# Performance work log

Measured on AMD Instinct MI355X. Metric: run time of the kernel, lower is better.

Reference implementation:

```python
import jax, jax.numpy as jnp
import numpy as np

# module config (matches init_kwargs)
NUM_CHIPS = 8
EPC = 8                 # experts_per_chip
E = 64                  # n_routed_experts = NUM_CHIPS * EPC
K = 4                   # num_experts_per_tok
META = 8                # metadata_len
M = 1024                # max_dispatched_tokens_per_expert
S = 512                 # seq_len_per_chip
H = 2048                # hidden_dim


def setup_inputs() -> dict:
    key = jax.random.key(0)
    k1, k2, k3 = jax.random.split(key, 3)
    x = jax.random.normal(k1, (NUM_CHIPS, S, H), jnp.float32)
    weights = jax.random.normal(k2, (NUM_CHIPS, S, K), jnp.float32)
    indices = jax.random.randint(k3, (NUM_CHIPS, S, K), 0, E, dtype=jnp.int32)
    return {"x": x, "weights": weights, "indices": indices}


def _local_ranks(f):
    # f: (S*K,) expert ids for one chip, in loop order (token-major, topk-minor).
    # rank[i] = number of earlier entries routed to the same expert.
    oh = (f[:, None] == jnp.arange(E)[None, :]).astype(jnp.int32)  # (SK, E)
    csum = jnp.cumsum(oh, axis=0)
    return jnp.take_along_axis(csum, f[:, None], axis=1)[:, 0] - 1


def reference(x, weights, indices):
    C, S_, K_ = indices.shape
    f = indices.reshape(C, S_ * K_)  # (C, SK) routed expert per dispatch entry

    # per-(chip, expert) token counts, then exclusive prefix-sum over chips -> base offsets
    counts = jax.vmap(lambda fi: jnp.zeros((E,), jnp.int32).at[fi].add(1))(f)  # (C, E)
    cum = jnp.cumsum(counts, axis=0)
    offset_base = jnp.concatenate([jnp.zeros((1, E), jnp.int32), cum[:-1]], axis=0)
    tokens_per_expert = cum[-1].reshape(NUM_CHIPS, EPC).astype(jnp.int32)

    # destination slot within each expert buffer = base offset + within-chip arrival rank
    rank = jax.vmap(_local_ranks)(f)                                 # (C, SK)
    dst = jnp.take_along_axis(offset_base, f, axis=1) + rank         # (C, SK)
    # expert_chip*EPC + expert_within_chip == routed_expert, so flat buffer row = f*M + dst
    slot = (f * M + dst).reshape(-1)                                 # (C*SK,)

    # scatter token hidden states
    x_entries = jnp.broadcast_to(x[:, :, None, :], (C, S_, K_, H)).reshape(-1, H)
    dispatched = (jnp.zeros((E * M, H), jnp.float32)
                  .at[slot].set(x_entries)
                  .reshape(NUM_CHIPS, EPC, M, H))

    # scatter metadata rows [chip, token, topk_idx, expert, int(weight), 0...]
    chip_ids = jnp.broadcast_to(jnp.arange(C)[:, None, None], (C, S_, K_)).reshape(-1)
    tok_ids = jnp.broadcast_to(jnp.arange(S_)[None, :, None], (C, S_, K_)).reshape(-1)
    k_ids = jnp.broadcast_to(jnp.arange(K_)[None, None, :], (C, S_, K_)).reshape(-1)
    w_int = weights.reshape(-1).astype(jnp.int32)  # original writes float into int32 buffer (truncates)
    meta_rows = jnp.stack([chip_ids, tok_ids, k_ids, f.reshape(-1), w_int], axis=1).astype(jnp.int32)
    meta_rows = jnp.concatenate(
        [meta_rows, jnp.zeros((meta_rows.shape[0], META - 5), jnp.int32)], axis=1)
    metadata = (jnp.full((E * M, META), -1, jnp.int32)
                .at[slot].set(meta_rows)
                .reshape(NUM_CHIPS, EPC, M, META))

    return dispatched, metadata, tokens_per_expert
```

## Files before the change

kernel.cpp:

```cpp
#include <hip/hip_runtime.h>

#define NUM_CHIPS 8
#define EPC 8
#define E_EXPERTS 64
#define TOPK 4
#define META 8
#define M_CAP 1024
#define SEQ 512
#define HID 2048
#define SK (SEQ * TOPK)
#define ROWS (E_EXPERTS * M_CAP)

#define DISP_SZ ((size_t)ROWS * HID)
#define META_OFF DISP_SZ
#define TOK_OFF (DISP_SZ + (size_t)ROWS * META)

#define WS_INV 0
#define WS_CNT (ROWS)
#define WS_OFB (ROWS + 512)
#define WS_TOT (ROWS + 1024)

typedef float vfloat4 __attribute__((ext_vector_type(4)));

__global__ __launch_bounds__(256) void count_kernel(const int* __restrict__ idx,
                                                    int* __restrict__ ws) {
    const int c = blockIdx.x;
    const int t = threadIdx.x;
    __shared__ __align__(16) unsigned char f[SK];
    __shared__ int partial[4][E_EXPERTS];

    const int* ic = idx + c * SK;
    for (int i = t; i < SK; i += 256) f[i] = (unsigned char)ic[i];
    __syncthreads();

    const int e = t & 63;
    const int q = t >> 6;
    const unsigned eb = (unsigned)e;
    const unsigned* fw = (const unsigned*)f;
    int cnt = 0;
    for (int w = q * 128; w < q * 128 + 128; ++w) {
        unsigned v = fw[w];
        cnt += ((v & 0xffu) == eb);
        cnt += (((v >> 8) & 0xffu) == eb);
        cnt += (((v >> 16) & 0xffu) == eb);
        cnt += ((v >> 24) == eb);
    }
    partial[q][e] = cnt;
    __syncthreads();
    if (q == 0) {
        int s = partial[0][e] + partial[1][e] + partial[2][e] + partial[3][e];
        ws[WS_CNT + c * E_EXPERTS + e] = s;
    }
}

__global__ void prefix_kernel(int* __restrict__ ws, float* __restrict__ out) {
    const int e = threadIdx.x;
    int base = 0;
    for (int c = 0; c < NUM_CHIPS; ++c) {
        ws[WS_OFB + c * E_EXPERTS + e] = base;
        base += ws[WS_CNT + c * E_EXPERTS + e];
    }
    ws[WS_TOT + e] = base;
    out[TOK_OFF + e] = (float)base;
}

__global__ __launch_bounds__(256) void rank_kernel(const int* __restrict__ idx,
                                                   int* __restrict__ ws) {
    const int c = blockIdx.x;
    const int t = threadIdx.x;
    __shared__ __align__(16) unsigned char f[SK];
    __shared__ int partial[4][E_EXPERTS];

    const int* ic = idx + c * SK;
    for (int i = t; i < SK; i += 256) f[i] = (unsigned char)ic[i];
    __syncthreads();

    const int e = t & 63;
    const int q = t >> 6;
    const unsigned eb = (unsigned)e;
    const unsigned* fw = (const unsigned*)f;
    int cnt = 0;
    for (int w = q * 128; w < q * 128 + 128; ++w) {
        unsigned v = fw[w];
        cnt += ((v & 0xffu) == eb);
        cnt += (((v >> 8) & 0xffu) == eb);
        cnt += (((v >> 16) & 0xffu) == eb);
        cnt += ((v >> 24) == eb);
    }
    partial[q][e] = cnt;
    __syncthreads();

    int base = ws[WS_OFB + c * E_EXPERTS + e];
    for (int qq = 0; qq < q; ++qq) base += partial[qq][e];

    int* inv = ws + WS_INV;
    for (int i = q * 512; i < q * 512 + 512; ++i) {
        if ((int)f[i] == e) {
            inv[e * M_CAP + base] = c * SK + i;
            ++base;
        }
    }
}

__global__ __launch_bounds__(256) void fill_kernel(const float* __restrict__ x,
                                                   const float* __restrict__ wts,
                                                   const int* __restrict__ ws,
                                                   float* __restrict__ out) {
    const int row = blockIdx.x;
    const int e = row >> 10;
    const int p = row & (M_CAP - 1);
    const int t = threadIdx.x;

    const int total = ws[WS_TOT + e];
    vfloat4* d4 = (vfloat4*)(out + (size_t)row * HID);
    float* meta = out + META_OFF + (size_t)row * META;

    if (p < total) {
        const int entry = ws[WS_INV + row];
        const int c = entry >> 11;
        const int i = entry & (SK - 1);
        const int tok = i >> 2;
        const int k = i & 3;
        const vfloat4* s4 = (const vfloat4*)(x + ((size_t)(c * SEQ + tok)) * HID);
        vfloat4 v0 = s4[t];
        vfloat4 v1 = s4[t + 256];
        __builtin_nontemporal_store(v0, d4 + t);
        __builtin_nontemporal_store(v1, d4 + t + 256);
        if (t < META) {
            float mv;
            if (t == 0)      mv = (float)c;
            else if (t == 1) mv = (float)tok;
            else if (t == 2) mv = (float)k;
            else if (t == 3) mv = (float)e;
            else if (t == 4) mv = (float)((int)wts[(c * SEQ + tok) * TOPK + k]);
            else             mv = 0.0f;
            meta[t] = mv;
        }
    } else {
        vfloat4 z = (vfloat4)(0.0f);
        __builtin_nontemporal_store(z, d4 + t);
        __builtin_nontemporal_store(z, d4 + t + 256);
        if (t < META) meta[t] = -1.0f;
    }
}

extern "C" void kernel_launch(void* const* d_in, const int* in_sizes, int n_in,
                              void* d_out, int out_size, void* d_ws, size_t ws_size,
                              hipStream_t stream) {
    const float* x   = (const float*)d_in[0];
    const float* wts = (const float*)d_in[1];
    const int* idx   = (const int*)d_in[2];
    float* out = (float*)d_out;
    int* ws = (int*)d_ws;

    count_kernel<<<NUM_CHIPS, 256, 0, stream>>>(idx, ws);
    prefix_kernel<<<1, 64, 0, stream>>>(ws, out);
    rank_kernel<<<NUM_CHIPS, 256, 0, stream>>>(idx, ws);
    fill_kernel<<<ROWS, 256, 0, stream>>>(x, wts, ws, out);
}
```

Measured before the change: 600.8 us.

## Zero-fill dispatch buffer with memset and launch copy blocks only for routed entries

```diff
diff --git a/kernel.cpp b/kernel.cpp
--- a/kernel.cpp
+++ b/kernel.cpp
@@ -10,15 +10,17 @@
 #define HID 2048
 #define SK (SEQ * TOPK)
 #define ROWS (E_EXPERTS * M_CAP)
+#define NENTRIES (NUM_CHIPS * SK)
 
 #define DISP_SZ ((size_t)ROWS * HID)
 #define META_OFF DISP_SZ
 #define TOK_OFF (DISP_SZ + (size_t)ROWS * META)
 
-#define WS_INV 0
-#define WS_CNT (ROWS)
-#define WS_OFB (ROWS + 512)
-#define WS_TOT (ROWS + 1024)
+#define WS_CNT 0
+#define WS_OFB 512
+#define WS_TOT 1024
+#define WS_GB  1088
+#define WS_DENSE 1152
 
 typedef float vfloat4 __attribute__((ext_vector_type(4)));
 
@@ -54,6 +56,7 @@
 }
 
 __global__ void prefix_kernel(int* __restrict__ ws, float* __restrict__ out) {
+    __shared__ int tot[E_EXPERTS];
     const int e = threadIdx.x;
     int base = 0;
     for (int c = 0; c < NUM_CHIPS; ++c) {
@@ -61,7 +64,12 @@
         base += ws[WS_CNT + c * E_EXPERTS + e];
     }
     ws[WS_TOT + e] = base;
+    tot[e] = base;
     out[TOK_OFF + e] = (float)base;
+    __syncthreads();
+    int g = 0;
+    for (int j = 0; j < e; ++j) g += tot[j];
+    ws[WS_GB + e] = g;
 }
 
 __global__ __launch_bounds__(256) void rank_kernel(const int* __restrict__ idx,
@@ -90,57 +98,57 @@
     partial[q][e] = cnt;
     __syncthreads();
 
-    int base = ws[WS_OFB + c * E_EXPERTS + e];
-    for (int qq = 0; qq < q; ++qq) base += partial[qq][e];
+    int dst = ws[WS_OFB + c * E_EXPERTS + e];
+    for (int qq = 0; qq < q; ++qq) dst += partial[qq][e];
+    const int gb = ws[WS_GB + e];
 
-    int* inv = ws + WS_INV;
+    int* dense = ws + WS_DENSE;
     for (int i = q * 512; i < q * 512 + 512; ++i) {
         if ((int)f[i] == e) {
-            inv[e * M_CAP + base] = c * SK + i;
-            ++base;
+            const int g = gb + dst;
+            dense[2 * g]     = e * M_CAP + dst;
+            dense[2 * g + 1] = c * SK + i;
+            ++dst;
         }
     }
 }
 
-__global__ __launch_bounds__(256) void fill_kernel(const float* __restrict__ x,
+__global__ __launch_bounds__(256) void meta_init_kernel(float* __restrict__ out) {
+    const int i = blockIdx.x * 256 + threadIdx.x;
+    vfloat4 m1 = (vfloat4)(-1.0f);
+    __builtin_nontemporal_store(m1, (vfloat4*)(out + META_OFF) + i);
+}
+
+__global__ __launch_bounds__(256) void copy_kernel(const float* __restrict__ x,
                                                    const float* __restrict__ wts,
                                                    const int* __restrict__ ws,
                                                    float* __restrict__ out) {
-    const int row = blockIdx.x;
-    const int e = row >> 10;
-    const int p = row & (M_CAP - 1);
+    const int g = blockIdx.x;
     const int t = threadIdx.x;
+    const int row   = ws[WS_DENSE + 2 * g];
+    const int entry = ws[WS_DENSE + 2 * g + 1];
 
-    const int total = ws[WS_TOT + e];
+    const int c = entry >> 11;
+    const int i = entry & (SK - 1);
+    const int tok = i >> 2;
+    const int k = i & 3;
+
+    const vfloat4* s4 = (const vfloat4*)(x + ((size_t)(c * SEQ + tok)) * HID);
     vfloat4* d4 = (vfloat4*)(out + (size_t)row * HID);
-    float* meta = out + META_OFF + (size_t)row * META;
+    vfloat4 v0 = s4[t];
+    vfloat4 v1 = s4[t + 256];
+    __builtin_nontemporal_store(v0, d4 + t);
+    __builtin_nontemporal_store(v1, d4 + t + 256);
 
-    if (p < total) {
-        const int entry = ws[WS_INV + row];
-        const int c = entry >> 11;
-        const int i = entry & (SK - 1);
-        const int tok = i >> 2;
-        const int k = i & 3;
-        const vfloat4* s4 = (const vfloat4*)(x + ((size_t)(c * SEQ + tok)) * HID);
-        vfloat4 v0 = s4[t];
-        vfloat4 v1 = s4[t + 256];
-        __builtin_nontemporal_store(v0, d4 + t);
-        __builtin_nontemporal_store(v1, d4 + t + 256);
-        if (t < META) {
-            float mv;
-            if (t == 0)      mv = (float)c;
-            else if (t == 1) mv = (float)tok;
-            else if (t == 2) mv = (float)k;
-            else if (t == 3) mv = (float)e;
-            else if (t == 4) mv = (float)((int)wts[(c * SEQ + tok) * TOPK + k]);
-            else             mv = 0.0f;
-            meta[t] = mv;
-        }
-    } else {
-        vfloat4 z = (vfloat4)(0.0f);
-        __builtin_nontemporal_store(z, d4 + t);
-        __builtin_nontemporal_store(z, d4 + t + 256);
-        if (t < META) meta[t] = -1.0f;
+    if (t < META) {
+        float mv;
+        if (t == 0)      mv = (float)c;
+        else if (t == 1) mv = (float)tok;
+        else if (t == 2) mv = (float)k;
+        else if (t == 3) mv = (float)(row >> 10);
+        else if (t == 4) mv = (float)((int)wts[(c * SEQ + tok) * TOPK + k]);
+        else             mv = 0.0f;
+        out[META_OFF + (size_t)row * META + t] = mv;
     }
 }
 
@@ -153,8 +161,11 @@
     float* out = (float*)d_out;
     int* ws = (int*)d_ws;
 
+    hipMemsetAsync(out, 0, DISP_SZ * sizeof(float), stream);
+
     count_kernel<<<NUM_CHIPS, 256, 0, stream>>>(idx, ws);
     prefix_kernel<<<1, 64, 0, stream>>>(ws, out);
     rank_kernel<<<NUM_CHIPS, 256, 0, stream>>>(idx, ws);
-    fill_kernel<<<ROWS, 256, 0, stream>>>(x, wts, ws, out);
+    meta_init_kernel<<<(ROWS * META / 4) / 256, 256, 0, stream>>>(out);
+    copy_kernel<<<NENTRIES, 256, 0, stream>>>(x, wts, ws, out);
 }
```

Measured after the change: 624.0 us. +3.9%, slower.
